# Performance work log

Hardware: AMD Instinct MI355X
Metric: run time of the kernel (lower is better)

The kernel has to match this reference:

```python
import jax, jax.numpy as jnp
import numpy as np

B, S = 8, 128
D_SENS, D_ACT, D_STR, D_ENC, DIM = 512, 32, 128, 128, 128
D_JOINT = D_STR + D_ENC  # 256


def _l2norm(x):
    return x / jnp.clip(jnp.linalg.norm(x, axis=-1, keepdims=True), 1e-12)


def _mlp(x, layers):
    # layers: list of (W, b); ReLU between layers, none on output
    n = len(layers)
    for i, (W, b) in enumerate(layers):
        x = x @ W + b
        if i < n - 1:
            x = jax.nn.relu(x)
    return x


def _meta_mlp(x, p):
    x = jax.nn.relu(x @ p['W1'] + p['b1'])
    x = jax.nn.relu(x @ p['W2'] + p['b2'])
    return x @ p['W3'] + p['b3']


def setup_inputs() -> dict:
    key = jax.random.key(0)
    it = iter(jax.random.split(key, 40))
    w = lambda shape, s=0.02: jax.random.normal(next(it), shape, jnp.float32) * s
    H = D_ACT * 4  # to_transitions hidden dim (default mlp_hidden_dim)
    return dict(
        sensory=jax.random.normal(next(it), (B, S, D_SENS), jnp.float32),
        actions=jax.random.normal(next(it), (B, S, D_ACT), jnp.float32),
        init_hidden=w((1, D_STR), 0.01),
        tW1=w((D_ACT, H)), tb1=w((H,)),
        tW2=w((H, H)), tb2=w((H,)),
        tW3=w((H, D_STR * D_STR)), tb3=w((D_STR * D_STR,)),
        enc_w=w((D_SENS, D_ENC)), enc_b=w((D_ENC,)),
        dec_w=w((D_ENC, D_SENS)), dec_b=w((D_SENS,)),
        q_w=w((D_JOINT, DIM)), k_w=w((D_JOINT, DIM)), v_w=w((D_JOINT, DIM)),
        mW1=w((DIM, 2 * DIM)), mb1=w((2 * DIM,)),
        mW2=w((2 * DIM, 2 * DIM)), mb2=w((2 * DIM,)),
        mW3=w((2 * DIM, DIM)), mb3=w((DIM,)),
        oW1=w((DIM, 2 * DIM)), ob1=w((2 * DIM,)),
        oW2=w((2 * DIM, 2 * DIM)), ob2=w((2 * DIM,)),
        oW3=w((2 * DIM, D_JOINT)), ob3=w((D_JOINT,)),
        sW1=w((2 * D_STR + 1, 2 * D_STR)), sb1=w((2 * D_STR,)),
        sW2=w((2 * D_STR, 2 * D_STR)), sb2=w((2 * D_STR,)),
        sW3=w((2 * D_STR, D_STR)), sb3=w((D_STR,)),
        integration_ratio=jnp.asarray(0.1, jnp.float32),
    )


def reference(sensory, actions, init_hidden, tW1, tb1, tW2, tb2, tW3, tb3,
              enc_w, enc_b, dec_w, dec_b, q_w, k_w, v_w,
              mW1, mb1, mW2, mb2, mW3, mb3,
              oW1, ob1, oW2, ob2, oW3, ob3,
              sW1, sb1, sW2, sb2, sW3, sb3, integration_ratio):
    mse = lambda a, b: jnp.mean((a - b) ** 2)

    # --- PathIntegration: actions -> transitions -> scripted RNN scan ---
    trans = _mlp(actions, [(tW1, tb1), (tW2, tb2), (tW3, tb3)])  # (B,S,ds*ds)
    trans = trans.reshape(B, S, D_STR, D_STR)
    h0 = jnp.broadcast_to(_l2norm(init_hidden), (B, D_STR))

    def step(h, T):  # h (B,ds), T (B,ds,ds)
        h = _l2norm(jax.nn.relu(jnp.einsum('bi,bij->bj', h, T)))
        return h, h

    _, hs = jax.lax.scan(step, h0, jnp.swapaxes(trans, 0, 1))
    structural = jnp.swapaxes(hs, 0, 1)  # (B,S,ds)

    # --- sensory encoder (Linear) ---
    encoded = sensory @ enc_w + enc_b  # (B,S,D_ENC)

    meta_params = {'W1': mW1, 'b1': mb1, 'W2': mW2, 'b2': mb2, 'W3': mW3, 'b3': mb3}

    def retrieve(s, e):
        joint = jnp.concatenate((s, e), axis=-1)
        q = joint @ q_w
        r = _meta_mlp(q, meta_params)
        out = _mlp(r, [(oW1, ob1), (oW2, ob2), (oW3, ob3)])
        return out[..., :D_STR], out[..., D_STR:]

    # generative branch
    dec_gen_s, dec_enc = retrieve(structural, jnp.zeros_like(encoded))
    generative_pred_loss = mse(sensory, dec_enc @ dec_w + dec_b)

    # relational branch (source calls retrieve(zeros, encoded) twice)
    dec_s1, _ = retrieve(jnp.zeros_like(structural), encoded)
    dec_s2, _ = retrieve(jnp.zeros_like(structural), encoded)
    relational_loss = mse(dec_s1, structural) + mse(dec_s2, structural)

    # consistency / inference correction
    corr_s, corr_e = retrieve(dec_gen_s, encoded)
    sse = jnp.sum((corr_e - encoded) ** 2, axis=-1, keepdims=True)  # (B,S,1)
    pred_var = _mlp(jnp.concatenate((corr_s, dec_gen_s, sse), axis=-1),
                    [(sW1, sb1), (sW2, sb2), (sW3, sb3)])
    inf_s = dec_gen_s + (corr_s - dec_gen_s) * integration_ratio * pred_var
    consistency_loss = mse(dec_gen_s, inf_s)

    final_s, inf_e = retrieve(inf_s, jnp.zeros_like(encoded))
    inference_pred_loss = mse(sensory, inf_e @ dec_w + dec_b)

    # per-sample fast-weight memory gradients (nested vmap(grad))
    store = jnp.concatenate((final_s, encoded), axis=-1)
    keys = store @ k_w
    values = store @ v_w

    def meta_loss(p, k, v):
        return jnp.mean((_meta_mlp(k, p) - v) ** 2)

    per_grad = jax.vmap(jax.vmap(jax.grad(meta_loss), in_axes=(None, 0, 0)),
                        in_axes=(None, 0, 0))
    g = per_grad(meta_params, keys, values)  # each leaf (B,S,*param_shape)

    total = (generative_pred_loss + relational_loss
             + consistency_loss + inference_pred_loss)  # all loss weights 1.0
    return (total, g['W1'], g['b1'], g['W2'], g['b2'], g['W3'], g['b3'])
```

## Files before the change

kernel.cpp:

```cpp
#include <hip/hip_runtime.h>
#include <hip/hip_bf16.h>

constexpr size_t OFF_W1 = 1;
constexpr size_t OFF_B1 = OFF_W1 + (size_t)1024*32768;
constexpr size_t OFF_W2 = OFF_B1 + (size_t)1024*256;
constexpr size_t OFF_B2 = OFF_W2 + (size_t)1024*65536;
constexpr size_t OFF_W3 = OFF_B2 + (size_t)1024*256;
constexpr size_t OFF_B3 = OFF_W3 + (size_t)1024*32768;

__device__ __forceinline__ void stage_rows(float* buf, const float* src, int ld,
                                           int row0, int rows, int t)
{
    int r = t >> 5; if (rows == 4) r &= 3;
    const int k4 = (t & 31) * 4;
    float4 v = make_float4(0.f,0.f,0.f,0.f);
    if (src) v = *(const float4*)&src[(size_t)(row0 + r)*ld + k4];
    *(float4*)&buf[r*128 + k4] = v;
}

__device__ __forceinline__ void layer_n256_r8(
    const float* __restrict__ W, const float* __restrict__ bias, int K,
    const float* __restrict__ x, int xs, float* __restrict__ y, int relu, int t)
{
    const int c4 = (t & 63) * 4;
    const int r0 = (t >> 6) * 2;
    float4 a0 = bias ? *(const float4*)&bias[c4] : make_float4(0.f,0.f,0.f,0.f);
    float4 a1 = a0;
    const float* x0 = x + r0 * xs;
    const float* x1 = x0 + xs;
    for (int k = 0; k < K; ++k) {
        float4 w = *(const float4*)&W[(size_t)k*256 + c4];
        float xa = x0[k], xb = x1[k];
        a0.x = fmaf(w.x, xa, a0.x); a0.y = fmaf(w.y, xa, a0.y);
        a0.z = fmaf(w.z, xa, a0.z); a0.w = fmaf(w.w, xa, a0.w);
        a1.x = fmaf(w.x, xb, a1.x); a1.y = fmaf(w.y, xb, a1.y);
        a1.z = fmaf(w.z, xb, a1.z); a1.w = fmaf(w.w, xb, a1.w);
    }
    if (relu) {
        a0.x=fmaxf(a0.x,0.f); a0.y=fmaxf(a0.y,0.f); a0.z=fmaxf(a0.z,0.f); a0.w=fmaxf(a0.w,0.f);
        a1.x=fmaxf(a1.x,0.f); a1.y=fmaxf(a1.y,0.f); a1.z=fmaxf(a1.z,0.f); a1.w=fmaxf(a1.w,0.f);
    }
    *(float4*)&y[r0*256 + c4] = a0;
    *(float4*)&y[(r0+1)*256 + c4] = a1;
}

__device__ __forceinline__ void layer_n256_r4(
    const float* __restrict__ W, const float* __restrict__ bias, int K,
    const float* __restrict__ x, int xs, float* __restrict__ y, int relu,
    const float* __restrict__ mask, int t)
{
    const int c4 = (t & 63) * 4;
    const int r = t >> 6;
    float4 a = bias ? *(const float4*)&bias[c4] : make_float4(0.f,0.f,0.f,0.f);
    const float* xr = x + r * xs;
    for (int k = 0; k < K; ++k) {
        float4 w = *(const float4*)&W[(size_t)k*256 + c4];
        float xa = xr[k];
        a.x = fmaf(w.x, xa, a.x); a.y = fmaf(w.y, xa, a.y);
        a.z = fmaf(w.z, xa, a.z); a.w = fmaf(w.w, xa, a.w);
    }
    if (relu) {
        a.x=fmaxf(a.x,0.f); a.y=fmaxf(a.y,0.f); a.z=fmaxf(a.z,0.f); a.w=fmaxf(a.w,0.f);
    }
    if (mask) {
        float4 m = *(const float4*)&mask[r*256 + c4];
        a.x = (m.x > 0.f) ? a.x : 0.f; a.y = (m.y > 0.f) ? a.y : 0.f;
        a.z = (m.z > 0.f) ? a.z : 0.f; a.w = (m.w > 0.f) ? a.w : 0.f;
    }
    *(float4*)&y[r*256 + c4] = a;
}

__device__ __forceinline__ void layer_n128(
    const float* __restrict__ W, const float* __restrict__ bias, int K,
    const float* __restrict__ x, int xs, float* __restrict__ y, int ys, int relu,
    int rows, int t)
{
    const int c4 = (t & 31) * 4;
    int r = t >> 5; if (rows == 4) r &= 3;
    float4 a = bias ? *(const float4*)&bias[c4] : make_float4(0.f,0.f,0.f,0.f);
    const float* xr = x + r * xs;
    for (int k = 0; k < K; ++k) {
        float4 w = *(const float4*)&W[(size_t)k*128 + c4];
        float xa = xr[k];
        a.x = fmaf(w.x, xa, a.x); a.y = fmaf(w.y, xa, a.y);
        a.z = fmaf(w.z, xa, a.z); a.w = fmaf(w.w, xa, a.w);
    }
    if (relu) {
        a.x=fmaxf(a.x,0.f); a.y=fmaxf(a.y,0.f); a.z=fmaxf(a.z,0.f); a.w=fmaxf(a.w,0.f);
    }
    *(float4*)&y[r*ys + c4] = a;
}

__device__ __forceinline__ void layer_n128_dual(
    const float* __restrict__ W,
    const float* __restrict__ xA, const float* __restrict__ xB,
    float* __restrict__ y, int rows, int t)
{
    const int c4 = (t & 31) * 4;
    int r = t >> 5; if (rows == 4) r &= 3;
    float4 a = make_float4(0.f,0.f,0.f,0.f);
    const float* xa_ = xA + r * 128;
    const float* xb_ = xB + r * 128;
    for (int k = 0; k < 128; ++k) {
        float4 w = *(const float4*)&W[(size_t)k*128 + c4];
        float v = xa_[k];
        a.x = fmaf(w.x, v, a.x); a.y = fmaf(w.y, v, a.y);
        a.z = fmaf(w.z, v, a.z); a.w = fmaf(w.w, v, a.w);
    }
    for (int k = 0; k < 128; ++k) {
        float4 w = *(const float4*)&W[(size_t)(128+k)*128 + c4];
        float v = xb_[k];
        a.x = fmaf(w.x, v, a.x); a.y = fmaf(w.y, v, a.y);
        a.z = fmaf(w.z, v, a.z); a.w = fmaf(w.w, v, a.w);
    }
    *(float4*)&y[r*128 + c4] = a;
}

__device__ __forceinline__ void gemm_k128_compute(
    const float* __restrict__ A, int lda, const float* __restrict__ W,
    const float* __restrict__ bias, int bias_mode, int N, int m0, int n0, int t,
    float* __restrict__ As, float4* __restrict__ acc)
{
    for (int l = t; l < 4096; l += 256) {
        int r = l >> 7, k = l & 127;
        As[k*36 + r] = A[(size_t)(m0 + r)*lda + k];
    }
    __syncthreads();
    const int c4 = (t & 63) * 4;
    const int r0 = (t >> 6) * 8;
    float4 bv;
    if (bias_mode == 0) {
        bv = *(const float4*)&bias[n0 + c4];
    } else {
        const int n = n0 + c4;
        const int j = n >> 7, i = n & 127;
        bv.x = bias[(size_t)(i+0)*128 + j];
        bv.y = bias[(size_t)(i+1)*128 + j];
        bv.z = bias[(size_t)(i+2)*128 + j];
        bv.w = bias[(size_t)(i+3)*128 + j];
    }
    #pragma unroll
    for (int i = 0; i < 8; ++i) acc[i] = bv;
    const float* Wp = W + (size_t)n0 + c4;
    #pragma unroll 4
    for (int k = 0; k < 128; ++k) {
        float4 w = *(const float4*)&Wp[(size_t)k*N];
        float a[8];
        *(float4*)&a[0] = *(const float4*)&As[k*36 + r0];
        *(float4*)&a[4] = *(const float4*)&As[k*36 + r0 + 4];
        #pragma unroll
        for (int i = 0; i < 8; ++i) {
            acc[i].x = fmaf(w.x, a[i], acc[i].x);
            acc[i].y = fmaf(w.y, a[i], acc[i].y);
            acc[i].z = fmaf(w.z, a[i], acc[i].z);
            acc[i].w = fmaf(w.w, a[i], acc[i].w);
        }
    }
}

__global__ __launch_bounds__(256) void gemm_k128_kernel(
    const float* __restrict__ A, int lda, const float* __restrict__ W,
    const float* __restrict__ bias, int bias_mode, float* __restrict__ C, int N)
{
    __shared__ float As[128*36];
    float4 acc[8];
    const int t = threadIdx.x;
    const int m0 = blockIdx.x * 32, n0 = blockIdx.y * 256;
    gemm_k128_compute(A, lda, W, bias, bias_mode, N, m0, n0, t, As, acc);
    const int c4 = (t & 63) * 4;
    const int r0 = (t >> 6) * 8;
    #pragma unroll
    for (int i = 0; i < 8; ++i)
        *(float4*)&C[(size_t)(m0 + r0 + i)*N + n0 + c4] = acc[i];
}

__device__ __forceinline__ void block_mse_commit(float s, float scale,
                                                 float* __restrict__ accum,
                                                 float* __restrict__ red, int t)
{
    #pragma unroll
    for (int off = 32; off > 0; off >>= 1) s += __shfl_down(s, off, 64);
    if ((t & 63) == 0) red[t >> 6] = s;
    __syncthreads();
    if (t == 0) atomicAdd(accum, (red[0]+red[1]+red[2]+red[3]) * scale);
}

__global__ __launch_bounds__(256) void prep_kernel(
    const float* __restrict__ tW3,
    const float* __restrict__ mW2, const float* __restrict__ mW3,
    const float* __restrict__ actions,
    const float* __restrict__ tW1, const float* __restrict__ tb1,
    const float* __restrict__ tW2, const float* __restrict__ tb2,
    const float* __restrict__ sensory,
    const float* __restrict__ enc_w, const float* __restrict__ enc_b,
    float* __restrict__ tW3T, float* __restrict__ T2, float* __restrict__ T3,
    float* __restrict__ acc, float* __restrict__ a2, float* __restrict__ encoded)
{
    __shared__ float smem[64*129];
    const int t = threadIdx.x;
    const int bid = blockIdx.x;
    if (bid < 256) {
        const int k = bid >> 1, i0 = (bid & 1) * 64;
        const size_t base = (size_t)k << 14;
        for (int l = t; l < 8192; l += 256) {
            int ii = l >> 7, jj = l & 127;
            smem[ii*129 + jj] = tW3[base + (size_t)(i0+ii)*128 + jj];
        }
        __syncthreads();
        for (int l = t; l < 8192; l += 256) {
            int jj = l >> 6, ii = l & 63;
            tW3T[base + (size_t)jj*128 + i0 + ii] = smem[ii*129 + jj];
        }
    } else if (bid < 512) {
        const int c = bid - 256;
        T2[(size_t)c*256 + t] = mW2[(size_t)t*256 + c];
    } else if (bid < 640) {
        const int c = bid - 512;
        T3[(size_t)c*256 + t] = mW3[(size_t)t*128 + c];
    } else if (bid == 640) {
        if (t < 16) acc[t] = 0.f;
    } else if (bid < 769) {
        float* bufAct = smem;
        float* ping   = smem + 256;
        float* pong   = smem + 1280;
        const int row0 = (bid - 641) * 8;
        if (t < 64) {
            int r = t >> 3, c4 = (t & 7) * 4;
            *(float4*)&bufAct[r*32 + c4] =
                *(const float4*)&actions[(size_t)(row0 + r)*32 + c4];
        }
        __syncthreads();
        layer_n128(tW1, tb1, 32, bufAct, 32, ping, 128, 1, 8, t);
        __syncthreads();
        layer_n128(tW2, tb2, 128, ping, 128, pong, 128, 1, 8, t);
        __syncthreads();
        {
            int r = t >> 5, c4 = (t & 31) * 4;
            *(float4*)&a2[(size_t)(row0 + r)*128 + c4] = *(const float4*)&pong[r*128 + c4];
        }
    } else {
        const int q = bid - 769;
        const int m0 = (q & 15) * 64, n0 = (q >> 4) * 64;
        float (*As)[65] = (float(*)[65])smem;
        float (*Ws)[65] = (float(*)[65])(smem + 16*65);
        const int tx = t & 15, ty = t >> 4;
        float a4[4][4] = {};
        for (int k0 = 0; k0 < 512; k0 += 16) {
            for (int l = t; l < 1024; l += 256) {
                int mm = l >> 4, kk = l & 15;
                As[kk][mm] = sensory[(size_t)(m0+mm)*512 + k0 + kk];
            }
            for (int l = t; l < 1024; l += 256) {
                int kk = l >> 6, nn = l & 63;
                Ws[kk][nn] = enc_w[(size_t)(k0+kk)*128 + n0 + nn];
            }
            __syncthreads();
            #pragma unroll
            for (int kk = 0; kk < 16; ++kk) {
                float a[4], b[4];
                #pragma unroll
                for (int i=0;i<4;i++) a[i] = As[kk][ty*4+i];
                #pragma unroll
                for (int j=0;j<4;j++) b[j] = Ws[kk][tx*4+j];
                #pragma unroll
                for (int i=0;i<4;i++)
                    #pragma unroll
                    for (int j=0;j<4;j++)
                        a4[i][j] = fmaf(a[i], b[j], a4[i][j]);
            }
            __syncthreads();
        }
        #pragma unroll
        for (int i=0;i<4;i++){
            int gm = m0 + ty*4 + i;
            #pragma unroll
            for (int j=0;j<4;j++){
                int gn = n0 + tx*4 + j;
                encoded[(size_t)gm*128 + gn] = a4[i][j] + enc_b[gn];
            }
        }
    }
}

__global__ __launch_bounds__(512) void scanrel_kernel(
    const float* __restrict__ transT,
    const float* __restrict__ init_hidden,
    float* __restrict__ structural,
    const float* __restrict__ encoded,
    const float* __restrict__ qw,
    const float* __restrict__ mW1, const float* __restrict__ mb1,
    const float* __restrict__ mW2, const float* __restrict__ mb2,
    const float* __restrict__ mW3, const float* __restrict__ mb3,
    const float* __restrict__ oW1, const float* __restrict__ ob1,
    const float* __restrict__ oW2, const float* __restrict__ ob2,
    const float* __restrict__ oW3, const float* __restrict__ ob3,
    float* __restrict__ out2)
{
    __shared__ float smem[5120];
    const int tid = threadIdx.x;
    if (blockIdx.x < 8) {
        float* h  = smem;
        float* ws = smem + 128;
        const int b = blockIdx.x;
        const int j = tid >> 2, p = tid & 3;
        const int i0 = p * 32;

        if (tid < 32) {
            float4 v = *(const float4*)&init_hidden[tid*4];
            float ss = v.x*v.x + v.y*v.y + v.z*v.z + v.w*v.w;
            ss += __shfl_xor(ss, 16); ss += __shfl_xor(ss, 8); ss += __shfl_xor(ss, 4);
            ss += __shfl_xor(ss, 2);  ss += __shfl_xor(ss, 1);
            float inv = 1.f / fmaxf(sqrtf(ss), 1e-12f);
            v.x *= inv; v.y *= inv; v.z *= inv; v.w *= inv;
            *(float4*)&h[tid*4] = v;
        }
        __syncthreads();

        const size_t bbase = ((size_t)b) << 21;
        const int lane_off = j*128 + i0;
        float4 cur[8], nxt[8];
        {
            const float* T0 = transT + bbase + lane_off;
            #pragma unroll
            for (int r = 0; r < 8; ++r) cur[r] = *(const float4*)&T0[r*4];
        }
        for (int t = 0; t < 128; ++t) {
            const int tn = (t < 127) ? t + 1 : 127;
            const float* Tn = transT + bbase + ((size_t)tn << 14) + lane_off;
            #pragma unroll
            for (int r = 0; r < 8; ++r) nxt[r] = *(const float4*)&Tn[r*4];

            float4 a = make_float4(0.f, 0.f, 0.f, 0.f);
            #pragma unroll
            for (int r = 0; r < 8; ++r) {
                float4 hv = *(const float4*)&h[i0 + r*4];
                a.x = fmaf(hv.x, cur[r].x, a.x);
                a.y = fmaf(hv.y, cur[r].y, a.y);
                a.z = fmaf(hv.z, cur[r].z, a.z);
                a.w = fmaf(hv.w, cur[r].w, a.w);
            }
            float s = (a.x + a.y) + (a.z + a.w);
            s += __shfl_xor(s, 1);
            s += __shfl_xor(s, 2);
            float v = fmaxf(s, 0.f);
            float q = v * v;
            q += __shfl_xor(q, 4);  q += __shfl_xor(q, 8);
            q += __shfl_xor(q, 16); q += __shfl_xor(q, 32);
            if ((tid & 63) == 0) ws[tid >> 6] = q;
            __syncthreads();
            float ss = ((ws[0]+ws[1]) + (ws[2]+ws[3])) + ((ws[4]+ws[5]) + (ws[6]+ws[7]));
            float inv = 1.f / fmaxf(sqrtf(ss), 1e-12f);
            float hv = v * inv;
            __syncthreads();
            if (p == 0) h[j] = hv;
            else if (p == 1) structural[(((size_t)(b*128 + t)) << 7) + j] = hv;
            __syncthreads();
            #pragma unroll
            for (int r = 0; r < 8; ++r) cur[r] = nxt[r];
        }
    } else {
        float* bufB = smem;
        float* ping = smem + 1024;
        float* pong = smem + 3072;
        const int row0 = (blockIdx.x - 8) * 8;
        const bool act = (tid < 256);
        const int t = tid;
        if (act) stage_rows(bufB, encoded, 128, row0, 8, t);
        __syncthreads();
        if (act) layer_n128(qw + (size_t)128*128, nullptr, 128, bufB, 128, ping, 128, 0, 8, t);
        __syncthreads();
        if (act) layer_n256_r8(mW1, mb1, 128, ping, 128, pong, 1, t);
        __syncthreads();
        if (act) layer_n256_r8(mW2, mb2, 256, pong, 256, ping, 1, t);
        __syncthreads();
        if (act) layer_n128(mW3, mb3, 256, ping, 256, pong, 128, 0, 8, t);
        __syncthreads();
        if (act) layer_n256_r8(oW1, ob1, 128, pong, 128, ping, 1, t);
        __syncthreads();
        if (act) layer_n256_r8(oW2, ob2, 256, ping, 256, pong, 1, t);
        __syncthreads();
        if (act) layer_n256_r8(oW3, ob3, 256, pong, 256, ping, 0, t);
        __syncthreads();
        if (act) {
            for (int e = t; e < 512; e += 256) {
                int r = e >> 6, c = (e & 63) * 4;
                *(float4*)&out2[(size_t)(row0+r)*256 + c] = *(const float4*)&ping[r*256 + c];
            }
        }
    }
}

__global__ __launch_bounds__(256) void genmse_kernel(
    const float* __restrict__ structural,
    const float* __restrict__ qw,
    const float* __restrict__ mW1, const float* __restrict__ mb1,
    const float* __restrict__ mW2, const float* __restrict__ mb2,
    const float* __restrict__ mW3, const float* __restrict__ mb3,
    const float* __restrict__ oW1, const float* __restrict__ ob1,
    const float* __restrict__ oW2, const float* __restrict__ ob2,
    const float* __restrict__ oW3, const float* __restrict__ ob3,
    float* __restrict__ out1,
    const float* __restrict__ out2,
    float* __restrict__ acc)
{
    __shared__ float smem[5120];
    const int t = threadIdx.x;
    if (blockIdx.x < 128) {
        float* bufA = smem;
        float* ping = smem + 1024;
        float* pong = smem + 3072;
        const int row0 = blockIdx.x * 8;
        stage_rows(bufA, structural, 128, row0, 8, t);
        __syncthreads();
        layer_n128(qw, nullptr, 128, bufA, 128, ping, 128, 0, 8, t);
        __syncthreads();
        layer_n256_r8(mW1, mb1, 128, ping, 128, pong, 1, t);
        __syncthreads();
        layer_n256_r8(mW2, mb2, 256, pong, 256, ping, 1, t);
        __syncthreads();
        layer_n128(mW3, mb3, 256, ping, 256, pong, 128, 0, 8, t);
        __syncthreads();
        layer_n256_r8(oW1, ob1, 128, pong, 128, ping, 1, t);
        __syncthreads();
        layer_n256_r8(oW2, ob2, 256, ping, 256, pong, 1, t);
        __syncthreads();
        layer_n256_r8(oW3, ob3, 256, pong, 256, ping, 0, t);
        __syncthreads();
        for (int e = t; e < 512; e += 256) {
            int r = e >> 6, c = (e & 63) * 4;
            *(float4*)&out1[(size_t)(row0+r)*256 + c] = *(const float4*)&ping[r*256 + c];
        }
    } else {
        const int m = blockIdx.x - 128;
        float s = 0.f;
        for (int jj = t; jj < 128; jj += 256) {
            float d = out2[(size_t)m*256 + jj] - structural[(size_t)m*128 + jj];
            s = fmaf(d, d, s);
        }
        block_mse_commit(s, 2.f/131072.f, acc + 1, smem, t);
    }
}

__global__ __launch_bounds__(256) void bigfuse_kernel(
    const float* __restrict__ out1, const float* __restrict__ encoded,
    const float* __restrict__ ratio_p,
    const float* __restrict__ qw,
    const float* __restrict__ mW1, const float* __restrict__ mb1,
    const float* __restrict__ mW2, const float* __restrict__ mb2,
    const float* __restrict__ mW3, const float* __restrict__ mb3,
    const float* __restrict__ oW1, const float* __restrict__ ob1,
    const float* __restrict__ oW2, const float* __restrict__ ob2,
    const float* __restrict__ oW3, const float* __restrict__ ob3,
    const float* __restrict__ sW1, const float* __restrict__ sb1,
    const float* __restrict__ sW2, const float* __restrict__ sb2,
    const float* __restrict__ sW3, const float* __restrict__ sb3,
    const float* __restrict__ sensory, const float* __restrict__ dec_w,
    const float* __restrict__ dec_b,
    float* __restrict__ out4, float* __restrict__ acc)
{
    __shared__ float smem[5200];
    const int t = threadIdx.x;
    if (blockIdx.x >= 256) {
        const int q = blockIdx.x - 256;
        const int m0 = (q & 31) * 32, n0 = (q >> 5) * 256;
        float4 a4[8];
        gemm_k128_compute(out1 + 128, 256, dec_w, dec_b, 0, 512, m0, n0, t, smem, a4);
        const int c4 = (t & 63) * 4;
        const int r0 = (t >> 6) * 8;
        float s = 0.f;
        #pragma unroll
        for (int i = 0; i < 8; ++i) {
            float4 rv = *(const float4*)&sensory[(size_t)(m0 + r0 + i)*512 + n0 + c4];
            float dx = a4[i].x - rv.x, dy = a4[i].y - rv.y;
            float dz = a4[i].z - rv.z, dw = a4[i].w - rv.w;
            s += dx*dx + dy*dy + dz*dz + dw*dw;
        }
        __syncthreads();
        block_mse_commit(s, 1.f/524288.f, acc + 0, smem, t);
        return;
    }
    float* out1_s = smem;
    float* enc_s  = smem + 512;
    float* out3_s = smem + 1024;
    float* ping   = smem + 2048;
    float* pong   = smem + 3072;
    float* pvar_s = smem + 4096;
    float* infs_s = smem + 4608;
    float* sse    = smem + 5120;
    float* red    = smem + 5124;
    const int row0 = blockIdx.x * 4;
    {
        int r = (t >> 5) & 3, k4 = (t & 31) * 4;
        *(float4*)&out1_s[r*128 + k4] = *(const float4*)&out1[(size_t)(row0+r)*256 + k4];
        *(float4*)&enc_s[r*128 + k4]  = *(const float4*)&encoded[(size_t)(row0+r)*128 + k4];
    }
    __syncthreads();
    layer_n128_dual(qw, out1_s, enc_s, ping, 4, t); __syncthreads();
    layer_n256_r4(mW1, mb1, 128, ping, 128, pong, 1, nullptr, t); __syncthreads();
    layer_n256_r4(mW2, mb2, 256, pong, 256, ping, 1, nullptr, t); __syncthreads();
    layer_n128(mW3, mb3, 256, ping, 256, pong, 128, 0, 4, t); __syncthreads();
    layer_n256_r4(oW1, ob1, 128, pong, 128, ping, 1, nullptr, t); __syncthreads();
    layer_n256_r4(oW2, ob2, 256, ping, 256, pong, 1, nullptr, t); __syncthreads();
    layer_n256_r4(oW3, ob3, 256, pong, 256, out3_s, 0, nullptr, t); __syncthreads();
    {
        int r = (t >> 5) & 3, k4 = (t & 31) * 4;
        float4 ce = *(const float4*)&out3_s[r*256 + 128 + k4];
        float4 en = *(const float4*)&enc_s[r*128 + k4];
        float dx = ce.x-en.x, dy = ce.y-en.y, dz = ce.z-en.z, dw = ce.w-en.w;
        float ss = dx*dx + dy*dy + dz*dz + dw*dw;
        ss += __shfl_xor(ss, 16); ss += __shfl_xor(ss, 8); ss += __shfl_xor(ss, 4);
        ss += __shfl_xor(ss, 2);  ss += __shfl_xor(ss, 1);
        if ((t & 31) == 0) sse[r] = ss;
    }
    __syncthreads();
    {
        const int c4 = (t & 63) * 4;
        const int r = t >> 6;
        float4 a = *(const float4*)&sb1[c4];
        for (int k = 0; k < 128; ++k) {
            float4 w = *(const float4*)&sW1[(size_t)k*256 + c4];
            float xa = out3_s[r*256 + k];
            a.x=fmaf(w.x,xa,a.x); a.y=fmaf(w.y,xa,a.y); a.z=fmaf(w.z,xa,a.z); a.w=fmaf(w.w,xa,a.w);
        }
        for (int k = 0; k < 128; ++k) {
            float4 w = *(const float4*)&sW1[(size_t)(128+k)*256 + c4];
            float xa = out1_s[r*128 + k];
            a.x=fmaf(w.x,xa,a.x); a.y=fmaf(w.y,xa,a.y); a.z=fmaf(w.z,xa,a.z); a.w=fmaf(w.w,xa,a.w);
        }
        {
            float4 w = *(const float4*)&sW1[(size_t)256*256 + c4];
            float xa = sse[r];
            a.x=fmaf(w.x,xa,a.x); a.y=fmaf(w.y,xa,a.y); a.z=fmaf(w.z,xa,a.z); a.w=fmaf(w.w,xa,a.w);
        }
        a.x=fmaxf(a.x,0.f); a.y=fmaxf(a.y,0.f); a.z=fmaxf(a.z,0.f); a.w=fmaxf(a.w,0.f);
        *(float4*)&ping[r*256 + c4] = a;
    }
    __syncthreads();
    layer_n256_r4(sW2, sb2, 256, ping, 256, pong, 1, nullptr, t); __syncthreads();
    layer_n128(sW3, sb3, 256, pong, 256, pvar_s, 128, 0, 4, t); __syncthreads();
    {
        float ratio = ratio_p[0];
        float ssum = 0.f;
        for (int e = t; e < 512; e += 256) {
            int r = e >> 7, j = e & 127;
            float dgs = out1_s[r*128 + j];
            float cs  = out3_s[r*256 + j];
            float pv  = pvar_s[r*128 + j];
            float delta = (cs - dgs) * ratio * pv;
            infs_s[r*128 + j] = dgs + delta;
            ssum = fmaf(delta, delta, ssum);
        }
        #pragma unroll
        for (int off = 32; off > 0; off >>= 1) ssum += __shfl_down(ssum, off, 64);
        if ((t & 63) == 0) red[t >> 6] = ssum;
    }
    __syncthreads();
    if (t == 0) atomicAdd(acc + 2, (red[0]+red[1]+red[2]+red[3]) * (1.f/131072.f));
    layer_n128(qw, nullptr, 128, infs_s, 128, ping, 128, 0, 4, t); __syncthreads();
    layer_n256_r4(mW1, mb1, 128, ping, 128, pong, 1, nullptr, t); __syncthreads();
    layer_n256_r4(mW2, mb2, 256, pong, 256, ping, 1, nullptr, t); __syncthreads();
    layer_n128(mW3, mb3, 256, ping, 256, pong, 128, 0, 4, t); __syncthreads();
    layer_n256_r4(oW1, ob1, 128, pong, 128, ping, 1, nullptr, t); __syncthreads();
    layer_n256_r4(oW2, ob2, 256, ping, 256, pong, 1, nullptr, t); __syncthreads();
    layer_n256_r4(oW3, ob3, 256, pong, 256, ping, 0, nullptr, t); __syncthreads();
    {
        int r = t >> 6, c4 = (t & 63) * 4;
        *(float4*)&out4[(size_t)(row0+r)*256 + c4] = *(const float4*)&ping[r*256 + c4];
    }
}

__global__ __launch_bounds__(256) void gradfuse_kernel(
    const float* __restrict__ out4, const float* __restrict__ encoded,
    const float* __restrict__ k_w, const float* __restrict__ v_w,
    const float* __restrict__ mW1, const float* __restrict__ mb1,
    const float* __restrict__ mW2, const float* __restrict__ mb2,
    const float* __restrict__ mW3, const float* __restrict__ mb3,
    const float* __restrict__ T2, const float* __restrict__ T3,
    const float* __restrict__ sensory, const float* __restrict__ dec_w,
    const float* __restrict__ dec_b,
    float* __restrict__ acc, float* __restrict__ out)
{
    __shared__ float smem[6656];
    const int t = threadIdx.x;
    if (blockIdx.x >= 256) {
        const int q = blockIdx.x - 256;
        const int m0 = (q & 31) * 32, n0 = (q >> 5) * 256;
        float4 a4[8];
        gemm_k128_compute(out4 + 128, 256, dec_w, dec_b, 0, 512, m0, n0, t, smem, a4);
        const int c4 = (t & 63) * 4;
        const int r0 = (t >> 6) * 8;
        float s = 0.f;
        #pragma unroll
        for (int i = 0; i < 8; ++i) {
            float4 rv = *(const float4*)&sensory[(size_t)(m0 + r0 + i)*512 + n0 + c4];
            float dx = a4[i].x - rv.x, dy = a4[i].y - rv.y;
            float dz = a4[i].z - rv.z, dw = a4[i].w - rv.w;
            s += dx*dx + dy*dy + dz*dz + dw*dw;
        }
        __syncthreads();
        block_mse_commit(s, 1.f/524288.f, acc + 3, smem, t);
        return;
    }
    float* bufA = smem;
    float* bufB = smem + 512;
    float* ks   = smem + 1024;
    float* vs   = smem + 1536;
    float* h1   = smem + 2048;
    float* h2   = smem + 3072;
    float* dob  = smem + 4096;
    float* dh2  = smem + 4608;
    float* dh1  = smem + 5632;
    const int row0 = blockIdx.x * 4;

    stage_rows(bufA, out4, 256, row0, 4, t);
    stage_rows(bufB, encoded, 128, row0, 4, t);
    __syncthreads();
    layer_n128_dual(k_w, bufA, bufB, ks, 4, t);
    layer_n128_dual(v_w, bufA, bufB, vs, 4, t);
    __syncthreads();
    layer_n256_r4(mW1, mb1, 128, ks, 128, h1, 1, nullptr, t);
    __syncthreads();
    layer_n256_r4(mW2, mb2, 256, h1, 256, h2, 1, nullptr, t);
    __syncthreads();
    layer_n128(mW3, mb3, 256, h2, 256, dob, 128, 0, 4, t);
    __syncthreads();
    for (int e = t; e < 512; e += 256)
        dob[e] = (dob[e] - vs[e]) * 0.015625f;
    __syncthreads();
    layer_n256_r4(T3, nullptr, 128, dob, 128, dh2, 0, h2, t);
    __syncthreads();
    layer_n256_r4(T2, nullptr, 256, dh2, 256, dh1, 0, h1, t);
    __syncthreads();

    #pragma unroll
    for (int r = 0; r < 4; ++r) {
        const size_t row = row0 + r;
        {
            const int c4 = (t & 63) * 4;
            const int i0 = (t >> 6) * 32;
            const float4 dv = *(const float4*)&dh1[r*256 + c4];
            float* p = out + OFF_W1 + row*32768;
            for (int i = i0; i < i0 + 32; ++i) {
                float kv = ks[r*128 + i];
                float4 o; o.x = kv*dv.x; o.y = kv*dv.y; o.z = kv*dv.z; o.w = kv*dv.w;
                *(float4*)&p[(size_t)i*256 + c4] = o;
            }
            out[OFF_B1 + row*256 + t] = dh1[r*256 + t];
        }
        {
            const int c4 = (t & 63) * 4;
            const int i0 = (t >> 6) * 64;
            const float4 dv = *(const float4*)&dh2[r*256 + c4];
            float* p = out + OFF_W2 + row*65536;
            for (int i = i0; i < i0 + 64; ++i) {
                float hv = h1[r*256 + i];
                float4 o; o.x = hv*dv.x; o.y = hv*dv.y; o.z = hv*dv.z; o.w = hv*dv.w;
                *(float4*)&p[(size_t)i*256 + c4] = o;
            }
            out[OFF_B2 + row*256 + t] = dh2[r*256 + t];
        }
        {
            const int c4 = (t & 31) * 4;
            const int i0 = (t >> 5) * 32;
            const float4 dv = *(const float4*)&dob[r*128 + c4];
            float* p = out + OFF_W3 + row*32768;
            for (int i = i0; i < i0 + 32; ++i) {
                float hv = h2[r*256 + i];
                float4 o; o.x = hv*dv.x; o.y = hv*dv.y; o.z = hv*dv.z; o.w = hv*dv.w;
                *(float4*)&p[(size_t)i*128 + c4] = o;
            }
            if (t < 128) out[OFF_B3 + row*128 + t] = dob[r*128 + t];
        }
    }
}

__global__ void total_kernel(const float* acc, float* out) {
    if (threadIdx.x == 0)
        out[0] = acc[0] + acc[1] + acc[2] + acc[3];
}

extern "C" void kernel_launch(void* const* d_in, const int* in_sizes, int n_in,
                              void* d_out, int out_size, void* d_ws, size_t ws_size,
                              hipStream_t stream)
{
    const float* sensory     = (const float*)d_in[0];
    const float* actions     = (const float*)d_in[1];
    const float* init_hidden = (const float*)d_in[2];
    const float* tW1 = (const float*)d_in[3];  const float* tb1 = (const float*)d_in[4];
    const float* tW2 = (const float*)d_in[5];  const float* tb2 = (const float*)d_in[6];
    const float* tW3 = (const float*)d_in[7];  const float* tb3 = (const float*)d_in[8];
    const float* enc_w = (const float*)d_in[9];  const float* enc_b = (const float*)d_in[10];
    const float* dec_w = (const float*)d_in[11]; const float* dec_b = (const float*)d_in[12];
    const float* q_w = (const float*)d_in[13];
    const float* k_w = (const float*)d_in[14];
    const float* v_w = (const float*)d_in[15];
    const float* mW1 = (const float*)d_in[16]; const float* mb1 = (const float*)d_in[17];
    const float* mW2 = (const float*)d_in[18]; const float* mb2 = (const float*)d_in[19];
    const float* mW3 = (const float*)d_in[20]; const float* mb3 = (const float*)d_in[21];
    const float* oW1 = (const float*)d_in[22]; const float* ob1 = (const float*)d_in[23];
    const float* oW2 = (const float*)d_in[24]; const float* ob2 = (const float*)d_in[25];
    const float* oW3 = (const float*)d_in[26]; const float* ob3 = (const float*)d_in[27];
    const float* sW1 = (const float*)d_in[28]; const float* sb1 = (const float*)d_in[29];
    const float* sW2 = (const float*)d_in[30]; const float* sb2 = (const float*)d_in[31];
    const float* sW3 = (const float*)d_in[32]; const float* sb3 = (const float*)d_in[33];
    const float* ratio = (const float*)d_in[34];
    float* out = (float*)d_out;

    float* Wsp = (float*)d_ws;
    float* acc   = Wsp;
    float* ALIAS = Wsp + 16;
    float* structural = ALIAS + 131072;
    float* out1 = ALIAS + 262144;
    float* out2 = ALIAS + 524288;
    float* out4 = ALIAS + 1048576;
    float* tW3T = ALIAS;
    size_t off = 16 + 2097152;
    float* a2      = Wsp + off; off += 131072;
    float* encoded = Wsp + off; off += 131072;
    float* transT  = Wsp + off; off += 16777216;
    float* T2      = Wsp + off; off += 65536;
    float* T3      = Wsp + off; off += 32768;

    prep_kernel<<<801, 256, 0, stream>>>(tW3, mW2, mW3, actions, tW1, tb1, tW2, tb2,
                                         sensory, enc_w, enc_b, tW3T, T2, T3,
                                         acc, a2, encoded);

    gemm_k128_kernel<<<dim3(32, 64), 256, 0, stream>>>(a2, 128, tW3T, tb3, 1, transT, 16384);

    scanrel_kernel<<<136, 512, 0, stream>>>(transT, init_hidden, structural, encoded,
        q_w, mW1, mb1, mW2, mb2, mW3, mb3, oW1, ob1, oW2, ob2, oW3, ob3, out2);

    genmse_kernel<<<1152, 256, 0, stream>>>(structural,
        q_w, mW1, mb1, mW2, mb2, mW3, mb3, oW1, ob1, oW2, ob2, oW3, ob3,
        out1, out2, acc);

    bigfuse_kernel<<<320, 256, 0, stream>>>(out1, encoded, ratio,
        q_w, mW1, mb1, mW2, mb2, mW3, mb3, oW1, ob1, oW2, ob2, oW3, ob3,
        sW1, sb1, sW2, sb2, sW3, sb3, sensory, dec_w, dec_b, out4, acc);

    gradfuse_kernel<<<320, 256, 0, stream>>>(out4, encoded, k_w, v_w,
        mW1, mb1, mW2, mb2, mW3, mb3, T2, T3, sensory, dec_w, dec_b, acc, out);

    total_kernel<<<1, 64, 0, stream>>>(acc, out);
}
```

Measured before the change: 1.337 ms.

## Fuse genmse, bigfuse and gradfuse into one per-row mega kernel

```diff
diff --git a/kernel.cpp b/kernel.cpp
--- a/kernel.cpp
+++ b/kernel.cpp
@@ -7,16 +7,6 @@
 constexpr size_t OFF_B2 = OFF_W2 + (size_t)1024*65536;
 constexpr size_t OFF_W3 = OFF_B2 + (size_t)1024*256;
 constexpr size_t OFF_B3 = OFF_W3 + (size_t)1024*32768;
-
-__device__ __forceinline__ void stage_rows(float* buf, const float* src, int ld,
-                                           int row0, int rows, int t)
-{
-    int r = t >> 5; if (rows == 4) r &= 3;
-    const int k4 = (t & 31) * 4;
-    float4 v = make_float4(0.f,0.f,0.f,0.f);
-    if (src) v = *(const float4*)&src[(size_t)(row0 + r)*ld + k4];
-    *(float4*)&buf[r*128 + k4] = v;
-}
 
 __device__ __forceinline__ void layer_n256_r8(
     const float* __restrict__ W, const float* __restrict__ bias, int K,
@@ -116,64 +106,6 @@
     *(float4*)&y[r*128 + c4] = a;
 }
 
-__device__ __forceinline__ void gemm_k128_compute(
-    const float* __restrict__ A, int lda, const float* __restrict__ W,
-    const float* __restrict__ bias, int bias_mode, int N, int m0, int n0, int t,
-    float* __restrict__ As, float4* __restrict__ acc)
-{
-    for (int l = t; l < 4096; l += 256) {
-        int r = l >> 7, k = l & 127;
-        As[k*36 + r] = A[(size_t)(m0 + r)*lda + k];
-    }
-    __syncthreads();
-    const int c4 = (t & 63) * 4;
-    const int r0 = (t >> 6) * 8;
-    float4 bv;
-    if (bias_mode == 0) {
-        bv = *(const float4*)&bias[n0 + c4];
-    } else {
-        const int n = n0 + c4;
-        const int j = n >> 7, i = n & 127;
-        bv.x = bias[(size_t)(i+0)*128 + j];
-        bv.y = bias[(size_t)(i+1)*128 + j];
-        bv.z = bias[(size_t)(i+2)*128 + j];
-        bv.w = bias[(size_t)(i+3)*128 + j];
-    }
-    #pragma unroll
-    for (int i = 0; i < 8; ++i) acc[i] = bv;
-    const float* Wp = W + (size_t)n0 + c4;
-    #pragma unroll 4
-    for (int k = 0; k < 128; ++k) {
-        float4 w = *(const float4*)&Wp[(size_t)k*N];
-        float a[8];
-        *(float4*)&a[0] = *(const float4*)&As[k*36 + r0];
-        *(float4*)&a[4] = *(const float4*)&As[k*36 + r0 + 4];
-        #pragma unroll
-        for (int i = 0; i < 8; ++i) {
-            acc[i].x = fmaf(w.x, a[i], acc[i].x);
-            acc[i].y = fmaf(w.y, a[i], acc[i].y);
-            acc[i].z = fmaf(w.z, a[i], acc[i].z);
-            acc[i].w = fmaf(w.w, a[i], acc[i].w);
-        }
-    }
-}
-
-__global__ __launch_bounds__(256) void gemm_k128_kernel(
-    const float* __restrict__ A, int lda, const float* __restrict__ W,
-    const float* __restrict__ bias, int bias_mode, float* __restrict__ C, int N)
-{
-    __shared__ float As[128*36];
-    float4 acc[8];
-    const int t = threadIdx.x;
-    const int m0 = blockIdx.x * 32, n0 = blockIdx.y * 256;
-    gemm_k128_compute(A, lda, W, bias, bias_mode, N, m0, n0, t, As, acc);
-    const int c4 = (t & 63) * 4;
-    const int r0 = (t >> 6) * 8;
-    #pragma unroll
-    for (int i = 0; i < 8; ++i)
-        *(float4*)&C[(size_t)(m0 + r0 + i)*N + n0 + c4] = acc[i];
-}
-
 __device__ __forceinline__ void block_mse_commit(float s, float scale,
                                                  float* __restrict__ accum,
                                                  float* __restrict__ red, int t)
@@ -183,6 +115,35 @@
     if ((t & 63) == 0) red[t >> 6] = s;
     __syncthreads();
     if (t == 0) atomicAdd(accum, (red[0]+red[1]+red[2]+red[3]) * scale);
+}
+
+__device__ __forceinline__ void dec_mse(
+    const float* __restrict__ ret,
+    const float* __restrict__ sensory, int row0,
+    const float* __restrict__ dec_w, const float* __restrict__ dec_b,
+    float* __restrict__ accum, float* __restrict__ red, int t)
+{
+    const int c4 = (t & 127) * 4;
+    const int rb = (t >> 7) * 2;
+    float4 a0 = *(const float4*)&dec_b[c4];
+    float4 a1 = a0;
+    const float* x0 = ret + rb*256 + 128;
+    const float* x1 = x0 + 256;
+    for (int k = 0; k < 128; ++k) {
+        float4 w = *(const float4*)&dec_w[(size_t)k*512 + c4];
+        float xa = x0[k], xb = x1[k];
+        a0.x = fmaf(w.x, xa, a0.x); a0.y = fmaf(w.y, xa, a0.y);
+        a0.z = fmaf(w.z, xa, a0.z); a0.w = fmaf(w.w, xa, a0.w);
+        a1.x = fmaf(w.x, xb, a1.x); a1.y = fmaf(w.y, xb, a1.y);
+        a1.z = fmaf(w.z, xb, a1.z); a1.w = fmaf(w.w, xb, a1.w);
+    }
+    float4 s0 = *(const float4*)&sensory[(size_t)(row0+rb)*512 + c4];
+    float4 s1 = *(const float4*)&sensory[(size_t)(row0+rb+1)*512 + c4];
+    float dx0 = a0.x-s0.x, dy0 = a0.y-s0.y, dz0 = a0.z-s0.z, dw0 = a0.w-s0.w;
+    float dx1 = a1.x-s1.x, dy1 = a1.y-s1.y, dz1 = a1.z-s1.z, dw1 = a1.w-s1.w;
+    float s = dx0*dx0 + dy0*dy0 + dz0*dz0 + dw0*dw0
+            + dx1*dx1 + dy1*dy1 + dz1*dz1 + dw1*dw1;
+    block_mse_commit(s, 1.f/524288.f, accum, red, t);
 }
 
 __global__ __launch_bounds__(256) void prep_kernel(
@@ -280,6 +241,52 @@
             }
         }
     }
+}
+
+__global__ __launch_bounds__(256) void gemm_k128_kernel(
+    const float* __restrict__ A, int lda, const float* __restrict__ W,
+    const float* __restrict__ bias, float* __restrict__ C, int N)
+{
+    __shared__ float As[128*36];
+    const int t = threadIdx.x;
+    const int m0 = blockIdx.x * 32, n0 = blockIdx.y * 256;
+    for (int l = t; l < 4096; l += 256) {
+        int r = l >> 7, k = l & 127;
+        As[k*36 + r] = A[(size_t)(m0 + r)*lda + k];
+    }
+    __syncthreads();
+    const int c4 = (t & 63) * 4;
+    const int r0 = (t >> 6) * 8;
+    float4 bv;
+    {
+        const int n = n0 + c4;
+        const int j = n >> 7, i = n & 127;
+        bv.x = bias[(size_t)(i+0)*128 + j];
+        bv.y = bias[(size_t)(i+1)*128 + j];
+        bv.z = bias[(size_t)(i+2)*128 + j];
+        bv.w = bias[(size_t)(i+3)*128 + j];
+    }
+    float4 acc[8];
+    #pragma unroll
+    for (int i = 0; i < 8; ++i) acc[i] = bv;
+    const float* Wp = W + (size_t)n0 + c4;
+    #pragma unroll 4
+    for (int k = 0; k < 128; ++k) {
+        float4 w = *(const float4*)&Wp[(size_t)k*N];
+        float a[8];
+        *(float4*)&a[0] = *(const float4*)&As[k*36 + r0];
+        *(float4*)&a[4] = *(const float4*)&As[k*36 + r0 + 4];
+        #pragma unroll
+        for (int i = 0; i < 8; ++i) {
+            acc[i].x = fmaf(w.x, a[i], acc[i].x);
+            acc[i].y = fmaf(w.y, a[i], acc[i].y);
+            acc[i].z = fmaf(w.z, a[i], acc[i].z);
+            acc[i].w = fmaf(w.w, a[i], acc[i].w);
+        }
+    }
+    #pragma unroll
+    for (int i = 0; i < 8; ++i)
+        *(float4*)&C[(size_t)(m0 + r0 + i)*N + n0 + c4] = acc[i];
 }
 
 __global__ __launch_bounds__(512) void scanrel_kernel(
@@ -365,7 +372,11 @@
         const int row0 = (blockIdx.x - 8) * 8;
         const bool act = (tid < 256);
         const int t = tid;
-        if (act) stage_rows(bufB, encoded, 128, row0, 8, t);
+        if (act) {
+            int r = t >> 5, k4 = (t & 31) * 4;
+            *(float4*)&bufB[r*128 + k4] =
+                *(const float4*)&encoded[(size_t)(row0 + r)*128 + k4];
+        }
         __syncthreads();
         if (act) layer_n128(qw + (size_t)128*128, nullptr, 128, bufB, 128, ping, 128, 0, 8, t);
         __syncthreads();
@@ -390,59 +401,9 @@
     }
 }
 
-__global__ __launch_bounds__(256) void genmse_kernel(
-    const float* __restrict__ structural,
-    const float* __restrict__ qw,
-    const float* __restrict__ mW1, const float* __restrict__ mb1,
-    const float* __restrict__ mW2, const float* __restrict__ mb2,
-    const float* __restrict__ mW3, const float* __restrict__ mb3,
-    const float* __restrict__ oW1, const float* __restrict__ ob1,
-    const float* __restrict__ oW2, const float* __restrict__ ob2,
-    const float* __restrict__ oW3, const float* __restrict__ ob3,
-    float* __restrict__ out1,
-    const float* __restrict__ out2,
-    float* __restrict__ acc)
-{
-    __shared__ float smem[5120];
-    const int t = threadIdx.x;
-    if (blockIdx.x < 128) {
-        float* bufA = smem;
-        float* ping = smem + 1024;
-        float* pong = smem + 3072;
-        const int row0 = blockIdx.x * 8;
-        stage_rows(bufA, structural, 128, row0, 8, t);
-        __syncthreads();
-        layer_n128(qw, nullptr, 128, bufA, 128, ping, 128, 0, 8, t);
-        __syncthreads();
-        layer_n256_r8(mW1, mb1, 128, ping, 128, pong, 1, t);
-        __syncthreads();
-        layer_n256_r8(mW2, mb2, 256, pong, 256, ping, 1, t);
-        __syncthreads();
-        layer_n128(mW3, mb3, 256, ping, 256, pong, 128, 0, 8, t);
-        __syncthreads();
-        layer_n256_r8(oW1, ob1, 128, pong, 128, ping, 1, t);
-        __syncthreads();
-        layer_n256_r8(oW2, ob2, 256, ping, 256, pong, 1, t);
-        __syncthreads();
-        layer_n256_r8(oW3, ob3, 256, pong, 256, ping, 0, t);
-        __syncthreads();
-        for (int e = t; e < 512; e += 256) {
-            int r = e >> 6, c = (e & 63) * 4;
-            *(float4*)&out1[(size_t)(row0+r)*256 + c] = *(const float4*)&ping[r*256 + c];
-        }
-    } else {
-        const int m = blockIdx.x - 128;
-        float s = 0.f;
-        for (int jj = t; jj < 128; jj += 256) {
-            float d = out2[(size_t)m*256 + jj] - structural[(size_t)m*128 + jj];
-            s = fmaf(d, d, s);
-        }
-        block_mse_commit(s, 2.f/131072.f, acc + 1, smem, t);
-    }
-}
-
-__global__ __launch_bounds__(256) void bigfuse_kernel(
-    const float* __restrict__ out1, const float* __restrict__ encoded,
+__global__ __launch_bounds__(256) void mega_kernel(
+    const float* __restrict__ structural, const float* __restrict__ encoded,
+    const float* __restrict__ out2, const float* __restrict__ sensory,
     const float* __restrict__ ratio_p,
     const float* __restrict__ qw,
     const float* __restrict__ mW1, const float* __restrict__ mb1,
@@ -454,48 +415,57 @@
     const float* __restrict__ sW1, const float* __restrict__ sb1,
     const float* __restrict__ sW2, const float* __restrict__ sb2,
     const float* __restrict__ sW3, const float* __restrict__ sb3,
-    const float* __restrict__ sensory, const float* __restrict__ dec_w,
-    const float* __restrict__ dec_b,
-    float* __restrict__ out4, float* __restrict__ acc)
-{
-    __shared__ float smem[5200];
+    const float* __restrict__ k_w, const float* __restrict__ v_w,
+    const float* __restrict__ T2, const float* __restrict__ T3,
+    const float* __restrict__ dec_w, const float* __restrict__ dec_b,
+    float* __restrict__ acc, float* __restrict__ out)
+{
+    __shared__ float smem[9736];
+    float* enc_s    = smem;
+    float* struct_s = smem + 512;
+    float* ping     = smem + 1024;
+    float* pong     = smem + 2048;
+    float* ret1     = smem + 3072;
+    float* xa128    = smem + 4096;
+    float* out3_s   = smem + 4608;
+    float* pvar_s   = smem + 5632;
+    float* infs_s   = smem + 6144;
+    float* ks       = smem + 6656;
+    float* vs       = smem + 7168;
+    float* h1       = smem + 7680;
+    float* h2       = smem + 8704;
+    float* sse      = smem + 9728;
+    float* red      = smem + 9732;
     const int t = threadIdx.x;
-    if (blockIdx.x >= 256) {
-        const int q = blockIdx.x - 256;
-        const int m0 = (q & 31) * 32, n0 = (q >> 5) * 256;
-        float4 a4[8];
-        gemm_k128_compute(out1 + 128, 256, dec_w, dec_b, 0, 512, m0, n0, t, smem, a4);
-        const int c4 = (t & 63) * 4;
-        const int r0 = (t >> 6) * 8;
-        float s = 0.f;
-        #pragma unroll
-        for (int i = 0; i < 8; ++i) {
-            float4 rv = *(const float4*)&sensory[(size_t)(m0 + r0 + i)*512 + n0 + c4];
-            float dx = a4[i].x - rv.x, dy = a4[i].y - rv.y;
-            float dz = a4[i].z - rv.z, dw = a4[i].w - rv.w;
-            s += dx*dx + dy*dy + dz*dz + dw*dw;
-        }
-        __syncthreads();
-        block_mse_commit(s, 1.f/524288.f, acc + 0, smem, t);
-        return;
-    }
-    float* out1_s = smem;
-    float* enc_s  = smem + 512;
-    float* out3_s = smem + 1024;
-    float* ping   = smem + 2048;
-    float* pong   = smem + 3072;
-    float* pvar_s = smem + 4096;
-    float* infs_s = smem + 4608;
-    float* sse    = smem + 5120;
-    float* red    = smem + 5124;
     const int row0 = blockIdx.x * 4;
+
     {
         int r = (t >> 5) & 3, k4 = (t & 31) * 4;
-        *(float4*)&out1_s[r*128 + k4] = *(const float4*)&out1[(size_t)(row0+r)*256 + k4];
-        *(float4*)&enc_s[r*128 + k4]  = *(const float4*)&encoded[(size_t)(row0+r)*128 + k4];
-    }
-    __syncthreads();
-    layer_n128_dual(qw, out1_s, enc_s, ping, 4, t); __syncthreads();
+        *(float4*)&struct_s[r*128 + k4] = *(const float4*)&structural[(size_t)(row0+r)*128 + k4];
+        *(float4*)&enc_s[r*128 + k4]    = *(const float4*)&encoded[(size_t)(row0+r)*128 + k4];
+    }
+    __syncthreads();
+    layer_n128(qw, nullptr, 128, struct_s, 128, ping, 128, 0, 4, t); __syncthreads();
+    layer_n256_r4(mW1, mb1, 128, ping, 128, pong, 1, nullptr, t); __syncthreads();
+    layer_n256_r4(mW2, mb2, 256, pong, 256, ping, 1, nullptr, t); __syncthreads();
+    layer_n128(mW3, mb3, 256, ping, 256, pong, 128, 0, 4, t); __syncthreads();
+    layer_n256_r4(oW1, ob1, 128, pong, 128, ping, 1, nullptr, t); __syncthreads();
+    layer_n256_r4(oW2, ob2, 256, ping, 256, pong, 1, nullptr, t); __syncthreads();
+    layer_n256_r4(oW3, ob3, 256, pong, 256, ret1, 0, nullptr, t); __syncthreads();
+    {
+        float relsum = 0.f;
+        for (int e = t; e < 512; e += 256) {
+            int r = e >> 7, c = e & 127;
+            xa128[e] = ret1[r*256 + c];
+            float d = out2[(size_t)(row0+r)*256 + c] - struct_s[r*128 + c];
+            relsum = fmaf(d, d, relsum);
+        }
+        block_mse_commit(relsum, 2.f/131072.f, acc + 1, red, t);
+    }
+    __syncthreads();
+    dec_mse(ret1, sensory, row0, dec_w, dec_b, acc + 0, red, t);
+    __syncthreads();
+    layer_n128_dual(qw, xa128, enc_s, ping, 4, t); __syncthreads();
     layer_n256_r4(mW1, mb1, 128, ping, 128, pong, 1, nullptr, t); __syncthreads();
     layer_n256_r4(mW2, mb2, 256, pong, 256, ping, 1, nullptr, t); __syncthreads();
     layer_n128(mW3, mb3, 256, ping, 256, pong, 128, 0, 4, t); __syncthreads();
@@ -524,7 +494,7 @@
         }
         for (int k = 0; k < 128; ++k) {
             float4 w = *(const float4*)&sW1[(size_t)(128+k)*256 + c4];
-            float xa = out1_s[r*128 + k];
+            float xa = xa128[r*128 + k];
             a.x=fmaf(w.x,xa,a.x); a.y=fmaf(w.y,xa,a.y); a.z=fmaf(w.z,xa,a.z); a.w=fmaf(w.w,xa,a.w);
         }
         {
@@ -543,80 +513,35 @@
         float ssum = 0.f;
         for (int e = t; e < 512; e += 256) {
             int r = e >> 7, j = e & 127;
-            float dgs = out1_s[r*128 + j];
+            float dgs = xa128[r*128 + j];
             float cs  = out3_s[r*256 + j];
             float pv  = pvar_s[r*128 + j];
             float delta = (cs - dgs) * ratio * pv;
             infs_s[r*128 + j] = dgs + delta;
             ssum = fmaf(delta, delta, ssum);
         }
-        #pragma unroll
-        for (int off = 32; off > 0; off >>= 1) ssum += __shfl_down(ssum, off, 64);
-        if ((t & 63) == 0) red[t >> 6] = ssum;
-    }
-    __syncthreads();
-    if (t == 0) atomicAdd(acc + 2, (red[0]+red[1]+red[2]+red[3]) * (1.f/131072.f));
+        block_mse_commit(ssum, 1.f/131072.f, acc + 2, red, t);
+    }
+    __syncthreads();
     layer_n128(qw, nullptr, 128, infs_s, 128, ping, 128, 0, 4, t); __syncthreads();
     layer_n256_r4(mW1, mb1, 128, ping, 128, pong, 1, nullptr, t); __syncthreads();
     layer_n256_r4(mW2, mb2, 256, pong, 256, ping, 1, nullptr, t); __syncthreads();
     layer_n128(mW3, mb3, 256, ping, 256, pong, 128, 0, 4, t); __syncthreads();
     layer_n256_r4(oW1, ob1, 128, pong, 128, ping, 1, nullptr, t); __syncthreads();
     layer_n256_r4(oW2, ob2, 256, ping, 256, pong, 1, nullptr, t); __syncthreads();
-    layer_n256_r4(oW3, ob3, 256, pong, 256, ping, 0, nullptr, t); __syncthreads();
-    {
-        int r = t >> 6, c4 = (t & 63) * 4;
-        *(float4*)&out4[(size_t)(row0+r)*256 + c4] = *(const float4*)&ping[r*256 + c4];
-    }
-}
-
-__global__ __launch_bounds__(256) void gradfuse_kernel(
-    const float* __restrict__ out4, const float* __restrict__ encoded,
-    const float* __restrict__ k_w, const float* __restrict__ v_w,
-    const float* __restrict__ mW1, const float* __restrict__ mb1,
-    const float* __restrict__ mW2, const float* __restrict__ mb2,
-    const float* __restrict__ mW3, const float* __restrict__ mb3,
-    const float* __restrict__ T2, const float* __restrict__ T3,
-    const float* __restrict__ sensory, const float* __restrict__ dec_w,
-    const float* __restrict__ dec_b,
-    float* __restrict__ acc, float* __restrict__ out)
-{
-    __shared__ float smem[6656];
-    const int t = threadIdx.x;
-    if (blockIdx.x >= 256) {
-        const int q = blockIdx.x - 256;
-        const int m0 = (q & 31) * 32, n0 = (q >> 5) * 256;
-        float4 a4[8];
-        gemm_k128_compute(out4 + 128, 256, dec_w, dec_b, 0, 512, m0, n0, t, smem, a4);
-        const int c4 = (t & 63) * 4;
-        const int r0 = (t >> 6) * 8;
-        float s = 0.f;
-        #pragma unroll
-        for (int i = 0; i < 8; ++i) {
-            float4 rv = *(const float4*)&sensory[(size_t)(m0 + r0 + i)*512 + n0 + c4];
-            float dx = a4[i].x - rv.x, dy = a4[i].y - rv.y;
-            float dz = a4[i].z - rv.z, dw = a4[i].w - rv.w;
-            s += dx*dx + dy*dy + dz*dz + dw*dw;
-        }
-        __syncthreads();
-        block_mse_commit(s, 1.f/524288.f, acc + 3, smem, t);
-        return;
-    }
-    float* bufA = smem;
-    float* bufB = smem + 512;
-    float* ks   = smem + 1024;
-    float* vs   = smem + 1536;
-    float* h1   = smem + 2048;
-    float* h2   = smem + 3072;
-    float* dob  = smem + 4096;
-    float* dh2  = smem + 4608;
-    float* dh1  = smem + 5632;
-    const int row0 = blockIdx.x * 4;
-
-    stage_rows(bufA, out4, 256, row0, 4, t);
-    stage_rows(bufB, encoded, 128, row0, 4, t);
-    __syncthreads();
-    layer_n128_dual(k_w, bufA, bufB, ks, 4, t);
-    layer_n128_dual(v_w, bufA, bufB, vs, 4, t);
+    layer_n256_r4(oW3, ob3, 256, pong, 256, ret1, 0, nullptr, t); __syncthreads();
+    dec_mse(ret1, sensory, row0, dec_w, dec_b, acc + 3, red, t);
+    __syncthreads();
+    for (int e = t; e < 512; e += 256) {
+        int r = e >> 7, c = e & 127;
+        xa128[e] = ret1[r*256 + c];
+    }
+    __syncthreads();
+    float* dob = pvar_s;
+    float* dh2 = out3_s;
+    float* dh1 = ping;
+    layer_n128_dual(k_w, xa128, enc_s, ks, 4, t);
+    layer_n128_dual(v_w, xa128, enc_s, vs, 4, t);
     __syncthreads();
     layer_n256_r4(mW1, mb1, 128, ks, 128, h1, 1, nullptr, t);
     __syncthreads();
@@ -631,7 +556,6 @@
     __syncthreads();
     layer_n256_r4(T2, nullptr, 256, dh2, 256, dh1, 0, h1, t);
     __syncthreads();
-
     #pragma unroll
     for (int r = 0; r < 4; ++r) {
         const size_t row = row0 + r;
@@ -710,9 +634,7 @@
     float* acc   = Wsp;
     float* ALIAS = Wsp + 16;
     float* structural = ALIAS + 131072;
-    float* out1 = ALIAS + 262144;
     float* out2 = ALIAS + 524288;
-    float* out4 = ALIAS + 1048576;
     float* tW3T = ALIAS;
     size_t off = 16 + 2097152;
     float* a2      = Wsp + off; off += 131072;
@@ -725,21 +647,14 @@
                                          sensory, enc_w, enc_b, tW3T, T2, T3,
                                          acc, a2, encoded);
 
-    gemm_k128_kernel<<<dim3(32, 64), 256, 0, stream>>>(a2, 128, tW3T, tb3, 1, transT, 16384);
+    gemm_k128_kernel<<<dim3(32, 64), 256, 0, stream>>>(a2, 128, tW3T, tb3, transT, 16384);
 
     scanrel_kernel<<<136, 512, 0, stream>>>(transT, init_hidden, structural, encoded,
         q_w, mW1, mb1, mW2, mb2, mW3, mb3, oW1, ob1, oW2, ob2, oW3, ob3, out2);
 
-    genmse_kernel<<<1152, 256, 0, stream>>>(structural,
+    mega_kernel<<<256, 256, 0, stream>>>(structural, encoded, out2, sensory, ratio,
         q_w, mW1, mb1, mW2, mb2, mW3, mb3, oW1, ob1, oW2, ob2, oW3, ob3,
-        out1, out2, acc);
-
-    bigfuse_kernel<<<320, 256, 0, stream>>>(out1, encoded, ratio,
-        q_w, mW1, mb1, mW2, mb2, mW3, mb3, oW1, ob1, oW2, ob2, oW3, ob3,
-        sW1, sb1, sW2, sb2, sW3, sb3, sensory, dec_w, dec_b, out4, acc);
-
-    gradfuse_kernel<<<320, 256, 0, stream>>>(out4, encoded, k_w, v_w,
-        mW1, mb1, mW2, mb2, mW3, mb3, T2, T3, sensory, dec_w, dec_b, acc, out);
+        sW1, sb1, sW2, sb2, sW3, sb3, k_w, v_w, T2, T3, dec_w, dec_b, acc, out);
 
     total_kernel<<<1, 64, 0, stream>>>(acc, out);
 }
```

New measurement: 1.321 ms. Within noise of the previous version (-1.2%).
